# Kernel tuning notes

Hardware: AMD Instinct MI355X
Metric: run time of the kernel (lower is better)

## Reference

```python
import jax, jax.numpy as jnp
import numpy as np

N_NODES = 2048
N_EDGES = 8192
EDGE_DIM = 10
EDGE_HIDDEN = 32
HID = 160


def nnconv(x, edge_index, edge_attr, w1, b1, w2, b2, root, bias):
    """PyG-style NNConv with aggr='mean'.
    x: [N, HID], edge_attr: [E, EDGE_DIM], edge_index: [2, E] (src, dst).
    Per-edge weight W_e = MLP(e) reshaped to [HID, HID]; message = x[src] @ W_e,
    mean-aggregated at dst, plus root transform and bias.
    """
    n = x.shape[0]
    h = jax.nn.relu(edge_attr @ w1 + b1)                     # [E, EDGE_HIDDEN]
    W = (h @ w2 + b2).reshape(-1, HID, HID)                  # [E, HID, HID]
    src, dst = edge_index[0], edge_index[1]
    msg = jnp.einsum('ei,eio->eo', x[src], W)                # [E, HID]
    summed = jax.ops.segment_sum(msg, dst, num_segments=n)   # [N, HID]
    cnt = jax.ops.segment_sum(jnp.ones((msg.shape[0],), x.dtype), dst,
                              num_segments=n)
    aggr = summed / jnp.maximum(cnt, 1.0)[:, None]           # mean; 0 for isolated
    return aggr + x @ root + bias


def setup_inputs() -> dict:
    key = jax.random.key(0)
    ks = jax.random.split(key, 16)
    s = 1.0 / np.sqrt(HID)
    se = 1.0 / np.sqrt(EDGE_DIM)
    sh = 1.0 / np.sqrt(EDGE_HIDDEN)
    inp = {
        'x': jax.random.normal(ks[0], (N_NODES, HID), jnp.float32),
        'edge_attr': jax.random.uniform(ks[1], (N_EDGES, EDGE_DIM), jnp.float32),
        # conv1 (subgraph_conv1) params
        'w1_a': jax.random.normal(ks[2], (EDGE_DIM, EDGE_HIDDEN), jnp.float32) * se,
        'b1_a': jnp.zeros((EDGE_HIDDEN,), jnp.float32),
        'w2_a': jax.random.normal(ks[3], (EDGE_HIDDEN, HID * HID), jnp.float32) * sh,
        'b2_a': jnp.zeros((HID * HID,), jnp.float32),
        'root_a': jax.random.normal(ks[4], (HID, HID), jnp.float32) * s,
        'bias_a': jnp.zeros((HID,), jnp.float32),
        # conv2 (subgraph_conv2, applied twice) params
        'w1_b': jax.random.normal(ks[5], (EDGE_DIM, EDGE_HIDDEN), jnp.float32) * se,
        'b1_b': jnp.zeros((EDGE_HIDDEN,), jnp.float32),
        'w2_b': jax.random.normal(ks[6], (EDGE_HIDDEN, HID * HID), jnp.float32) * sh,
        'b2_b': jnp.zeros((HID * HID,), jnp.float32),
        'root_b': jax.random.normal(ks[7], (HID, HID), jnp.float32) * s,
        'bias_b': jnp.zeros((HID,), jnp.float32),
        'edge_index': jax.random.randint(ks[8], (2, N_EDGES), 0, N_NODES, jnp.int64),
    }
    return inp


def reference(x, edge_attr, w1_a, b1_a, w2_a, b2_a, root_a, bias_a,
              w1_b, b1_b, w2_b, b2_b, root_b, bias_b, edge_index):
    # subgraph_conv1 -> ReLU -> subgraph_conv2 -> ReLU -> subgraph_conv2
    h = jax.nn.relu(nnconv(x, edge_index, edge_attr,
                           w1_a, b1_a, w2_a, b2_a, root_a, bias_a))
    h = jax.nn.relu(nnconv(h, edge_index, edge_attr,
                           w1_b, b1_b, w2_b, b2_b, root_b, bias_b))
    h = nnconv(h, edge_index, edge_attr,
               w1_b, b1_b, w2_b, b2_b, root_b, bias_b)
    return h
```

## Files before the change

kernel.cpp:

```cpp
#include <hip/hip_runtime.h>

#define NN 2048
#define NE 8192
#define ED 10
#define EH 32
#define HID 160
#define NCOL 5504

typedef __attribute__((ext_vector_type(8))) short short8;
typedef __attribute__((ext_vector_type(4))) float f32x4;
typedef unsigned int u32;

__device__ __forceinline__ void split_bf16(float v, ushort& hi, ushort& lo) {
    unsigned u = __float_as_uint(v);
    hi = (ushort)(u >> 16);
    float hf = __uint_as_float(u & 0xffff0000u);
    lo = (ushort)(__float_as_uint(v - hf) >> 16);
}

__device__ __forceinline__ void gl2lds16(const ushort* g, ushort* l) {
    __builtin_amdgcn_global_load_lds(
        (const __attribute__((address_space(1))) u32*)g,
        (__attribute__((address_space(3))) u32*)l, 16, 0, 0);
}

__global__ void k_cvt(const float* __restrict__ x, ushort* __restrict__ xh,
                      ushort* __restrict__ xl) {
    int i = blockIdx.x * 256 + threadIdx.x;
    if (i >= NN * HID) return;
    ushort h, l; split_bf16(x[i], h, l);
    xh[i] = h; xl[i] = l;
}

__global__ void k_h2(const float* __restrict__ ea,
                     const float* __restrict__ w1a, const float* __restrict__ b1a,
                     const float* __restrict__ w1b, const float* __restrict__ b1b,
                     float* __restrict__ ha, float* __restrict__ hb) {
    int idx = blockIdx.x * 256 + threadIdx.x;
    if (idx >= NE * EH) return;
    const float* w1 = blockIdx.y ? w1b : w1a;
    const float* b1 = blockIdx.y ? b1b : b1a;
    float* h = blockIdx.y ? hb : ha;
    int e = idx >> 5, j = idx & 31;
    float acc = b1[j];
#pragma unroll
    for (int i = 0; i < ED; ++i) acc += ea[e * ED + i] * w1[i * EH + j];
    h[idx] = fmaxf(acc, 0.f);
}

__global__ void k_prepB2(const float* __restrict__ w2a, const float* __restrict__ b2a,
                         const float* __restrict__ roota,
                         const float* __restrict__ w2b, const float* __restrict__ b2b,
                         const float* __restrict__ rootb,
                         ushort* __restrict__ BhA, ushort* __restrict__ BlA,
                         ushort* __restrict__ BhB, ushort* __restrict__ BlB) {
    int idx = blockIdx.x * 256 + threadIdx.x;
    if (idx >= NCOL * HID) return;
    const float* w2 = blockIdx.y ? w2b : w2a;
    const float* b2 = blockIdx.y ? b2b : b2a;
    const float* root = blockIdx.y ? rootb : roota;
    ushort* Bh = blockIdx.y ? BhB : BhA;
    ushort* Bl = blockIdx.y ? BlB : BlA;
    int k = idx / NCOL;
    int n = idx - k * NCOL;
    float v;
    if (n < 5120) {
        int q = n / HID, o = n - q * HID;
        v = w2[q * (HID * HID) + k * HID + o];
    } else if (n < 5280) {
        v = b2[k * HID + (n - 5120)];
    } else if (n < 5440) {
        v = root[k * HID + (n - 5280)];
    } else {
        v = 0.f;
    }
    ushort h, l; split_bf16(v, h, l);
    Bh[(size_t)n * HID + k] = h;
    Bl[(size_t)n * HID + k] = l;
}

__global__ void k_zi(int* p, int n) {
    int i = blockIdx.x * 256 + threadIdx.x;
    if (i < n) p[i] = 0;
}
__global__ void k_count(const int* __restrict__ ei, int* __restrict__ degd,
                        int* __restrict__ dego) {
    int e = blockIdx.x * 256 + threadIdx.x;
    if (e < NE) {
        atomicAdd(&degd[ei[NE + e]], 1);
        atomicAdd(&dego[ei[e]], 1);
    }
}
__global__ void k_scan(const int* __restrict__ dego, const int* __restrict__ degd,
                       int* __restrict__ soff, int* __restrict__ cursor,
                       float* __restrict__ dinv) {
    __shared__ int ps[256];
    int t = threadIdx.x;
    int loc[8], s = 0;
#pragma unroll
    for (int i = 0; i < 8; ++i) { loc[i] = s; s += dego[t * 8 + i]; }
    ps[t] = s;
    __syncthreads();
    int total = s;
    for (int st = 1; st < 256; st <<= 1) {
        int v = (t >= st) ? ps[t - st] : 0;
        __syncthreads();
        ps[t] += v;
        __syncthreads();
    }
    int base = ps[t] - total;
#pragma unroll
    for (int i = 0; i < 8; ++i) {
        int b = t * 8 + i;
        soff[b] = base + loc[i];
        cursor[b] = base + loc[i];
        dinv[b] = 1.0f / fmaxf((float)degd[b], 1.0f);
    }
}
__global__ void k_fill(const int* __restrict__ ei, int* __restrict__ cursor,
                       int* __restrict__ selist) {
    int e = blockIdx.x * 256 + threadIdx.x;
    if (e < NE) {
        int s = ei[e];
        int p = atomicAdd(&cursor[s], 1);
        selist[p] = e;
    }
}

__global__ __launch_bounds__(256) void k_gemm(const ushort* __restrict__ Ah,
        const ushort* __restrict__ Al, const ushort* __restrict__ Bh,
        const ushort* __restrict__ Bl, float* __restrict__ G) {
    __shared__ ushort sAh[128 * 32], sAl[128 * 32], sBh[128 * 32], sBl[128 * 32];
    int tid = threadIdx.x;
    int bn = blockIdx.x * 128, bm = blockIdx.y * 128;
    int wid = tid >> 6, lane = tid & 63;
    int wm = (wid >> 1) * 64, wn = (wid & 1) * 64;
    int lr = lane & 15, lk = lane >> 4;
    f32x4 acc[4][4];
#pragma unroll
    for (int i = 0; i < 4; ++i)
#pragma unroll
        for (int j = 0; j < 4; ++j) acc[i][j] = (f32x4){0.f, 0.f, 0.f, 0.f};

    for (int c = 0; c < 5; ++c) {
        int k0 = c * 32;
#pragma unroll
        for (int i = 0; i < 2; ++i) {
            int s = tid + i * 256;
            int r = s >> 2, go = (s & 3) * 8;
            gl2lds16(&Ah[(size_t)(bm + r) * HID + k0 + go], &sAh[s * 8]);
            gl2lds16(&Al[(size_t)(bm + r) * HID + k0 + go], &sAl[s * 8]);
            gl2lds16(&Bh[(size_t)(bn + r) * HID + k0 + go], &sBh[s * 8]);
            gl2lds16(&Bl[(size_t)(bn + r) * HID + k0 + go], &sBl[s * 8]);
        }
        __syncthreads();
        short8 ah[4], al[4];
#pragma unroll
        for (int mt = 0; mt < 4; ++mt) {
            int r = wm + mt * 16 + lr;
            ah[mt] = *(const short8*)&sAh[r * 32 + lk * 8];
            al[mt] = *(const short8*)&sAl[r * 32 + lk * 8];
        }
#pragma unroll
        for (int nt = 0; nt < 4; ++nt) {
            int r = wn + nt * 16 + lr;
            short8 bh = *(const short8*)&sBh[r * 32 + lk * 8];
            short8 bl = *(const short8*)&sBl[r * 32 + lk * 8];
#pragma unroll
            for (int mt = 0; mt < 4; ++mt) {
                acc[mt][nt] = __builtin_amdgcn_mfma_f32_16x16x32_bf16(ah[mt], bh, acc[mt][nt], 0, 0, 0);
                acc[mt][nt] = __builtin_amdgcn_mfma_f32_16x16x32_bf16(ah[mt], bl, acc[mt][nt], 0, 0, 0);
                acc[mt][nt] = __builtin_amdgcn_mfma_f32_16x16x32_bf16(al[mt], bh, acc[mt][nt], 0, 0, 0);
            }
        }
        __syncthreads();
    }
#pragma unroll
    for (int mt = 0; mt < 4; ++mt)
#pragma unroll
        for (int nt = 0; nt < 4; ++nt) {
            int m0 = bm + wm + mt * 16 + lk * 4;
            int n = bn + wn + nt * 16 + lr;
#pragma unroll
            for (int r = 0; r < 4; ++r)
                G[(size_t)(m0 + r) * NCOL + n] = acc[mt][nt][r];
        }
}

__global__ void k_aggr(const float* __restrict__ G, const float* __restrict__ h,
                       const int* __restrict__ ei, const int* __restrict__ soff,
                       const int* __restrict__ dego, const int* __restrict__ selist,
                       float* __restrict__ sumb) {
    __shared__ float Gs[5280];
    int s = blockIdx.x, t = threadIdx.x;
    const float4* Grow = (const float4*)(G + (size_t)s * NCOL);
    for (int k = t; k < 1320; k += 160)
        ((float4*)Gs)[k] = Grow[k];
    __syncthreads();
    int o0 = soff[s], dg = dego[s];
    for (int j = 0; j < dg; ++j) {
        int e = selist[o0 + j];
        int dst = ei[NE + e];
        const float4* hp = (const float4*)(h + e * EH);
        float a = Gs[5120 + t];
#pragma unroll
        for (int qq = 0; qq < 8; ++qq) {
            float4 hv = hp[qq];
            a += hv.x * Gs[(qq * 4 + 0) * HID + t];
            a += hv.y * Gs[(qq * 4 + 1) * HID + t];
            a += hv.z * Gs[(qq * 4 + 2) * HID + t];
            a += hv.w * Gs[(qq * 4 + 3) * HID + t];
        }
        atomicAdd(&sumb[dst * HID + t], a);
    }
}

__global__ void k_final(float* __restrict__ sumb, const float* __restrict__ G,
                        const float* __restrict__ dinv, const float* __restrict__ bias,
                        float* __restrict__ outf, ushort* __restrict__ oh,
                        ushort* __restrict__ ol, int relu_cvt) {
    int idx = blockIdx.x * 256 + threadIdx.x;
    if (idx >= NN * HID) return;
    int d = idx / HID, o = idx - d * HID;
    float sv = sumb[idx];
    sumb[idx] = 0.f;
    float v = sv * dinv[d] + G[(size_t)d * NCOL + 5280 + o] + bias[o];
    if (relu_cvt) {
        v = fmaxf(v, 0.f);
        ushort hi, lo; split_bf16(v, hi, lo);
        oh[idx] = hi;
        ol[idx] = lo;
    } else {
        outf[idx] = v;
    }
}

extern "C" void kernel_launch(void* const* d_in, const int* in_sizes, int n_in,
                              void* d_out, int out_size, void* d_ws, size_t ws_size,
                              hipStream_t stream) {
    const float* x     = (const float*)d_in[0];
    const float* ea    = (const float*)d_in[1];
    const float* w1a   = (const float*)d_in[2];
    const float* b1a   = (const float*)d_in[3];
    const float* w2a   = (const float*)d_in[4];
    const float* b2a   = (const float*)d_in[5];
    const float* roota = (const float*)d_in[6];
    const float* biasa = (const float*)d_in[7];
    const float* w1b   = (const float*)d_in[8];
    const float* b1b   = (const float*)d_in[9];
    const float* w2b   = (const float*)d_in[10];
    const float* b2b   = (const float*)d_in[11];
    const float* rootb = (const float*)d_in[12];
    const float* biasb = (const float*)d_in[13];
    const int*   ei    = (const int*)d_in[14];
    float* out = (float*)d_out;

    char* p = (char*)d_ws;
    float* G = (float*)p;          p += (size_t)NN * NCOL * 4;
    float* sumb = (float*)p;       p += (size_t)NN * HID * 4;
    int* degd = (int*)p;           p += NN * 4;
    int* dego = (int*)p;           p += NN * 4;
    ushort* BhA = (ushort*)p;      p += (size_t)NCOL * HID * 2;
    ushort* BlA = (ushort*)p;      p += (size_t)NCOL * HID * 2;
    ushort* BhB = (ushort*)p;      p += (size_t)NCOL * HID * 2;
    ushort* BlB = (ushort*)p;      p += (size_t)NCOL * HID * 2;
    float* h_a = (float*)p;        p += (size_t)NE * EH * 4;
    float* h_b = (float*)p;        p += (size_t)NE * EH * 4;
    ushort* xh = (ushort*)p;       p += (size_t)NN * HID * 2;
    ushort* xl = (ushort*)p;       p += (size_t)NN * HID * 2;
    int* soff = (int*)p;           p += NN * 4;
    int* cursor = (int*)p;         p += NN * 4;
    float* dinv = (float*)p;       p += NN * 4;
    int* selist = (int*)p;         p += NE * 4;

    k_cvt<<<(NN * HID) / 256, 256, 0, stream>>>(x, xh, xl);
    k_prepB2<<<dim3((NCOL * HID) / 256, 2), 256, 0, stream>>>(
        w2a, b2a, roota, w2b, b2b, rootb, BhA, BlA, BhB, BlB);
    k_h2<<<dim3((NE * EH) / 256, 2), 256, 0, stream>>>(ea, w1a, b1a, w1b, b1b, h_a, h_b);
    k_zi<<<(NN * HID + 2 * NN) / 256, 256, 0, stream>>>((int*)sumb, NN * HID + 2 * NN);
    k_count<<<NE / 256, 256, 0, stream>>>(ei, degd, dego);
    k_scan<<<1, 256, 0, stream>>>(dego, degd, soff, cursor, dinv);
    k_fill<<<NE / 256, 256, 0, stream>>>(ei, cursor, selist);

    struct Layer { const ushort *bh, *bl; const float *h, *bias; int relu; };
    Layer L[3] = {
        {BhA, BlA, h_a, biasa, 1},
        {BhB, BlB, h_b, biasb, 1},
        {BhB, BlB, h_b, biasb, 0},
    };
    for (int l = 0; l < 3; ++l) {
        k_gemm<<<dim3(NCOL / 128, NN / 128), 256, 0, stream>>>(xh, xl, L[l].bh, L[l].bl, G);
        k_aggr<<<NN, HID, 0, stream>>>(G, L[l].h, ei, soff, dego, selist, sumb);
        k_final<<<(NN * HID) / 256, 256, 0, stream>>>(sumb, G, dinv, L[l].bias, out,
                                                      xh, xl, L[l].relu);
    }
}
```

Baseline: 240.2 us.

## Merge prep kernels, build CSR in one block, keep full B tile in LDS

Folds the x conversion, the sumb zeroing and the edge-MLP hidden computation into one launch. Replaces the separate count, scan and fill kernels with a single 1024-thread block that builds the CSR in shared memory. The GEMM now loads the whole 128x160 B tile (hi and lo) into LDS once and reads A fragments straight from global memory, removing the per-chunk barriers. The risks are the serial single-block CSR build and uncoalesced global A loads. The selist order from atomics stays nondeterministic, as before.

```diff
diff --git a/kernel.cpp b/kernel.cpp
--- a/kernel.cpp
+++ b/kernel.cpp
@@ -24,23 +24,25 @@
         (__attribute__((address_space(3))) u32*)l, 16, 0, 0);
 }
 
-__global__ void k_cvt(const float* __restrict__ x, ushort* __restrict__ xh,
-                      ushort* __restrict__ xl) {
-    int i = blockIdx.x * 256 + threadIdx.x;
-    if (i >= NN * HID) return;
-    ushort h, l; split_bf16(x[i], h, l);
-    xh[i] = h; xl[i] = l;
-}
-
-__global__ void k_h2(const float* __restrict__ ea,
-                     const float* __restrict__ w1a, const float* __restrict__ b1a,
-                     const float* __restrict__ w1b, const float* __restrict__ b1b,
-                     float* __restrict__ ha, float* __restrict__ hb) {
-    int idx = blockIdx.x * 256 + threadIdx.x;
-    if (idx >= NE * EH) return;
-    const float* w1 = blockIdx.y ? w1b : w1a;
-    const float* b1 = blockIdx.y ? b1b : b1a;
-    float* h = blockIdx.y ? hb : ha;
+__global__ void k_prep(const float* __restrict__ x, ushort* __restrict__ xh,
+                       ushort* __restrict__ xl, float* __restrict__ sumb,
+                       const float* __restrict__ ea,
+                       const float* __restrict__ w1a, const float* __restrict__ b1a,
+                       const float* __restrict__ w1b, const float* __restrict__ b1b,
+                       float* __restrict__ ha, float* __restrict__ hb) {
+    int b = blockIdx.x, t = threadIdx.x;
+    if (b < 1280) {
+        int i = b * 256 + t;
+        ushort h, l; split_bf16(x[i], h, l);
+        xh[i] = h; xl[i] = l;
+        sumb[i] = 0.f;
+        return;
+    }
+    int isB = (b >= 2304);
+    int idx = (b - (isB ? 2304 : 1280)) * 256 + t;
+    const float* w1 = isB ? w1b : w1a;
+    const float* b1 = isB ? b1b : b1a;
+    float* h = isB ? hb : ha;
     int e = idx >> 5, j = idx & 31;
     float acc = b1[j];
 #pragma unroll
@@ -79,50 +81,40 @@
     Bl[(size_t)n * HID + k] = l;
 }
 
-__global__ void k_zi(int* p, int n) {
-    int i = blockIdx.x * 256 + threadIdx.x;
-    if (i < n) p[i] = 0;
-}
-__global__ void k_count(const int* __restrict__ ei, int* __restrict__ degd,
-                        int* __restrict__ dego) {
-    int e = blockIdx.x * 256 + threadIdx.x;
-    if (e < NE) {
+__global__ __launch_bounds__(1024) void k_csr(const int* __restrict__ ei,
+                                              int* __restrict__ soff,
+                                              int* __restrict__ dego_g,
+                                              float* __restrict__ dinv,
+                                              int* __restrict__ selist) {
+    __shared__ int degd[NN], dego[NN], cur[NN], part[1024];
+    int t = threadIdx.x;
+    degd[t] = 0; degd[t + 1024] = 0;
+    dego[t] = 0; dego[t + 1024] = 0;
+    __syncthreads();
+    for (int e = t; e < NE; e += 1024) {
         atomicAdd(&degd[ei[NE + e]], 1);
         atomicAdd(&dego[ei[e]], 1);
     }
-}
-__global__ void k_scan(const int* __restrict__ dego, const int* __restrict__ degd,
-                       int* __restrict__ soff, int* __restrict__ cursor,
-                       float* __restrict__ dinv) {
-    __shared__ int ps[256];
-    int t = threadIdx.x;
-    int loc[8], s = 0;
-#pragma unroll
-    for (int i = 0; i < 8; ++i) { loc[i] = s; s += dego[t * 8 + i]; }
-    ps[t] = s;
-    __syncthreads();
-    int total = s;
-    for (int st = 1; st < 256; st <<= 1) {
-        int v = (t >= st) ? ps[t - st] : 0;
+    __syncthreads();
+    int a0 = dego[2 * t], a1 = dego[2 * t + 1];
+    part[t] = a0 + a1;
+    __syncthreads();
+    for (int st = 1; st < 1024; st <<= 1) {
+        int v = (t >= st) ? part[t - st] : 0;
         __syncthreads();
-        ps[t] += v;
+        part[t] += v;
         __syncthreads();
     }
-    int base = ps[t] - total;
-#pragma unroll
-    for (int i = 0; i < 8; ++i) {
-        int b = t * 8 + i;
-        soff[b] = base + loc[i];
-        cursor[b] = base + loc[i];
-        dinv[b] = 1.0f / fmaxf((float)degd[b], 1.0f);
-    }
-}
-__global__ void k_fill(const int* __restrict__ ei, int* __restrict__ cursor,
-                       int* __restrict__ selist) {
-    int e = blockIdx.x * 256 + threadIdx.x;
-    if (e < NE) {
+    int base = part[t] - (a0 + a1);
+    soff[2 * t] = base;       cur[2 * t] = base;
+    soff[2 * t + 1] = base + a0; cur[2 * t + 1] = base + a0;
+    dego_g[2 * t] = a0;       dego_g[2 * t + 1] = a1;
+    dinv[2 * t] = 1.0f / fmaxf((float)degd[2 * t], 1.0f);
+    dinv[2 * t + 1] = 1.0f / fmaxf((float)degd[2 * t + 1], 1.0f);
+    __syncthreads();
+    for (int e = t; e < NE; e += 1024) {
         int s = ei[e];
-        int p = atomicAdd(&cursor[s], 1);
+        int p = atomicAdd(&cur[s], 1);
         selist[p] = e;
     }
 }
@@ -130,9 +122,21 @@
 __global__ __launch_bounds__(256) void k_gemm(const ushort* __restrict__ Ah,
         const ushort* __restrict__ Al, const ushort* __restrict__ Bh,
         const ushort* __restrict__ Bl, float* __restrict__ G) {
-    __shared__ ushort sAh[128 * 32], sAl[128 * 32], sBh[128 * 32], sBl[128 * 32];
+    __shared__ ushort sBh[128 * HID], sBl[128 * HID];
     int tid = threadIdx.x;
     int bn = blockIdx.x * 128, bm = blockIdx.y * 128;
+#pragma unroll
+    for (int i = 0; i < 10; ++i) {
+        int s = tid + i * 256;
+        int r = s / 20, j = s - r * 20;
+        gl2lds16(&Bh[(size_t)(bn + r) * HID + j * 8], &sBh[s * 8]);
+    }
+#pragma unroll
+    for (int i = 0; i < 10; ++i) {
+        int s = tid + i * 256;
+        int r = s / 20, j = s - r * 20;
+        gl2lds16(&Bl[(size_t)(bn + r) * HID + j * 8], &sBl[s * 8]);
+    }
     int wid = tid >> 6, lane = tid & 63;
     int wm = (wid >> 1) * 64, wn = (wid & 1) * 64;
     int lr = lane & 15, lk = lane >> 4;
@@ -141,31 +145,22 @@
     for (int i = 0; i < 4; ++i)
 #pragma unroll
         for (int j = 0; j < 4; ++j) acc[i][j] = (f32x4){0.f, 0.f, 0.f, 0.f};
+    __syncthreads();
 
     for (int c = 0; c < 5; ++c) {
         int k0 = c * 32;
-#pragma unroll
-        for (int i = 0; i < 2; ++i) {
-            int s = tid + i * 256;
-            int r = s >> 2, go = (s & 3) * 8;
-            gl2lds16(&Ah[(size_t)(bm + r) * HID + k0 + go], &sAh[s * 8]);
-            gl2lds16(&Al[(size_t)(bm + r) * HID + k0 + go], &sAl[s * 8]);
-            gl2lds16(&Bh[(size_t)(bn + r) * HID + k0 + go], &sBh[s * 8]);
-            gl2lds16(&Bl[(size_t)(bn + r) * HID + k0 + go], &sBl[s * 8]);
-        }
-        __syncthreads();
         short8 ah[4], al[4];
 #pragma unroll
         for (int mt = 0; mt < 4; ++mt) {
-            int r = wm + mt * 16 + lr;
-            ah[mt] = *(const short8*)&sAh[r * 32 + lk * 8];
-            al[mt] = *(const short8*)&sAl[r * 32 + lk * 8];
+            size_t off = (size_t)(bm + wm + mt * 16 + lr) * HID + k0 + lk * 8;
+            ah[mt] = *(const short8*)&Ah[off];
+            al[mt] = *(const short8*)&Al[off];
         }
 #pragma unroll
         for (int nt = 0; nt < 4; ++nt) {
-            int r = wn + nt * 16 + lr;
-            short8 bh = *(const short8*)&sBh[r * 32 + lk * 8];
-            short8 bl = *(const short8*)&sBl[r * 32 + lk * 8];
+            int rr = wn + nt * 16 + lr;
+            short8 bh = *(const short8*)&sBh[rr * HID + k0 + lk * 8];
+            short8 bl = *(const short8*)&sBl[rr * HID + k0 + lk * 8];
 #pragma unroll
             for (int mt = 0; mt < 4; ++mt) {
                 acc[mt][nt] = __builtin_amdgcn_mfma_f32_16x16x32_bf16(ah[mt], bh, acc[mt][nt], 0, 0, 0);
@@ -173,7 +168,6 @@
                 acc[mt][nt] = __builtin_amdgcn_mfma_f32_16x16x32_bf16(al[mt], bh, acc[mt][nt], 0, 0, 0);
             }
         }
-        __syncthreads();
     }
 #pragma unroll
     for (int mt = 0; mt < 4; ++mt)
@@ -258,8 +252,6 @@
     char* p = (char*)d_ws;
     float* G = (float*)p;          p += (size_t)NN * NCOL * 4;
     float* sumb = (float*)p;       p += (size_t)NN * HID * 4;
-    int* degd = (int*)p;           p += NN * 4;
-    int* dego = (int*)p;           p += NN * 4;
     ushort* BhA = (ushort*)p;      p += (size_t)NCOL * HID * 2;
     ushort* BlA = (ushort*)p;      p += (size_t)NCOL * HID * 2;
     ushort* BhB = (ushort*)p;      p += (size_t)NCOL * HID * 2;
@@ -269,18 +261,14 @@
     ushort* xh = (ushort*)p;       p += (size_t)NN * HID * 2;
     ushort* xl = (ushort*)p;       p += (size_t)NN * HID * 2;
     int* soff = (int*)p;           p += NN * 4;
-    int* cursor = (int*)p;         p += NN * 4;
+    int* dego = (int*)p;           p += NN * 4;
     float* dinv = (float*)p;       p += NN * 4;
     int* selist = (int*)p;         p += NE * 4;
 
-    k_cvt<<<(NN * HID) / 256, 256, 0, stream>>>(x, xh, xl);
+    k_prep<<<3328, 256, 0, stream>>>(x, xh, xl, sumb, ea, w1a, b1a, w1b, b1b, h_a, h_b);
     k_prepB2<<<dim3((NCOL * HID) / 256, 2), 256, 0, stream>>>(
         w2a, b2a, roota, w2b, b2b, rootb, BhA, BlA, BhB, BlB);
-    k_h2<<<dim3((NE * EH) / 256, 2), 256, 0, stream>>>(ea, w1a, b1a, w1b, b1b, h_a, h_b);
-    k_zi<<<(NN * HID + 2 * NN) / 256, 256, 0, stream>>>((int*)sumb, NN * HID + 2 * NN);
-    k_count<<<NE / 256, 256, 0, stream>>>(ei, degd, dego);
-    k_scan<<<1, 256, 0, stream>>>(dego, degd, soff, cursor, dinv);
-    k_fill<<<NE / 256, 256, 0, stream>>>(ei, cursor, selist);
+    k_csr<<<1, 1024, 0, stream>>>(ei, soff, dego, dinv, selist);
 
     struct Layer { const ushort *bh, *bl; const float *h, *bias; int relu; };
     Layer L[3] = {
```

Measured after the change: 248.3 us. +3.4%, slower.
